# Kernel tuning notes

Measured on AMD Instinct MI355X. Metric: run time of the kernel, lower is better.

The kernel has to match this reference:

```python
import jax, jax.numpy as jnp
import numpy as np

CAPACITY = 0.7
TEMP = 0.5          # initial_temp, never annealed (global_step=None path)
LB_WEIGHT = 0.005
Z_WEIGHT = 5e-06
EPS = 1e-10


def setup_inputs() -> dict:
    key = jax.random.key(0)
    k1, k2, k3 = jax.random.split(key, 3)
    B, S, H = 4, 8192, 2048
    return {
        "hidden_states": jax.random.normal(k1, (B, S, H), dtype=jnp.float32),
        "active_mask": jnp.ones((B, S), dtype=bool),
        "u": jax.random.uniform(k2, (B, S), dtype=jnp.float32),
        # router: nn.Linear(H, 1), weight ~ N(0, 0.02), bias = 0
        "w": jax.random.normal(k3, (H,), dtype=jnp.float32) * 0.02,
        "b": jnp.zeros((), dtype=jnp.float32),
    }


def reference(hidden_states, active_mask, u, w, b):
    B, S = active_mask.shape
    N = B * S
    # mask is all-True by construction -> num_active = N, k static
    num_active = N
    k = max(1, min(int(CAPACITY * num_active), num_active))

    # scores = router(hidden).squeeze(-1)  -> [B,S]
    scores = jnp.einsum("bsh,h->bs", hidden_states, w) + b
    scores = jnp.where(active_mask, scores, -jnp.inf)

    # gumbel noise from uniform u (matches torch.rand_like path)
    gumbel = -jnp.log(-jnp.log(u + EPS) + EPS)
    noisy = ((scores + gumbel) / TEMP).reshape(-1)  # [N]

    _, idx = jax.lax.top_k(noisy, k)
    ffn_mask = jnp.zeros((N,), dtype=bool).at[idx].set(True)
    ffn_mask = ffn_mask.reshape(B, S) & active_mask

    # aux losses (masked reductions over active tokens)
    maskf = active_mask.astype(jnp.float32)
    na = maskf.sum()
    safe_scores = jnp.where(active_mask, scores, 0.0)
    f = ffn_mask.astype(jnp.float32).sum() / na
    p = (jax.nn.sigmoid(safe_scores) * maskf).sum() / na
    lb_loss = (f - CAPACITY) ** 2 + (p - CAPACITY) ** 2
    z_loss = (safe_scores ** 2 * maskf).sum() / na
    aux_loss = LB_WEIGHT * lb_loss + Z_WEIGHT * z_loss

    return ffn_mask, aux_loss
```

## Files before the change

### kernel.cpp

```cpp
#include <hip/hip_runtime.h>
#include <math.h>

#define NTOK 32768
#define HDIM 2048
#define K_SEL 22937
#define EPS_F 1e-10f
#define SBLK 1024

__global__ void zero_kernel(uint4* __restrict__ h4)
{
    h4[blockIdx.x * 256 + threadIdx.x] = make_uint4(0u, 0u, 0u, 0u);
}

__global__ __launch_bounds__(256) void score_kernel(
    const float* __restrict__ hidden,
    const float* __restrict__ u,
    const float* __restrict__ w,
    const float* __restrict__ b,
    unsigned int* __restrict__ keys,
    float* __restrict__ pp,
    float* __restrict__ zz,
    unsigned int* __restrict__ hist,
    int shift)
{
    const int wave = threadIdx.x >> 6;
    const int lane = threadIdx.x & 63;
    const int row0 = blockIdx.x * 32 + wave * 8;

    const float4* __restrict__ w4 = (const float4*)w;
    float4 wr[8];
    #pragma unroll
    for (int j = 0; j < 8; ++j) wr[j] = w4[j * 64 + lane];

    const float4* __restrict__ rowp = (const float4*)(hidden + (size_t)row0 * HDIM);

    float sums[8];
    float4 buf[2][8];
    #pragma unroll
    for (int j = 0; j < 8; ++j) buf[0][j] = rowp[j * 64 + lane];

    #pragma unroll
    for (int r = 0; r < 8; ++r) {
        const int cur = r & 1, nxt = cur ^ 1;
        if (r < 7) {
            #pragma unroll
            for (int j = 0; j < 8; ++j)
                buf[nxt][j] = rowp[(r + 1) * 512 + j * 64 + lane];
        }
        float s = 0.0f;
        #pragma unroll
        for (int j = 0; j < 8; ++j) {
            const float4 hv = buf[cur][j];
            s += hv.x * wr[j].x + hv.y * wr[j].y + hv.z * wr[j].z + hv.w * wr[j].w;
        }
        sums[r] = s;
    }

    #pragma unroll
    for (int off = 32; off > 0; off >>= 1) {
        #pragma unroll
        for (int r = 0; r < 8; ++r)
            sums[r] += __shfl_down(sums[r], off, 64);
    }

    __shared__ float red_p[4], red_z[4];
    if (lane == 0) {
        const float bias = b[0];
        float p_acc = 0.0f, z_acc = 0.0f;
        #pragma unroll
        for (int r = 0; r < 8; ++r) {
            const float score = sums[r] + bias;
            const float uu = u[row0 + r];
            const float g = -logf(-logf(uu + EPS_F) + EPS_F);
            const float noisy = (score + g) * 2.0f;
            const unsigned int bits = __float_as_uint(noisy);
            const unsigned int k = (bits & 0x80000000u) ? ~bits : (bits | 0x80000000u);
            keys[row0 + r] = k;
            atomicAdd(&hist[k >> shift], 1u);
            p_acc += 1.0f / (1.0f + expf(-score));
            z_acc += score * score;
        }
        red_p[wave] = p_acc;
        red_z[wave] = z_acc;
    }
    __syncthreads();
    if (threadIdx.x == 0) {
        pp[blockIdx.x] = red_p[0] + red_p[1] + red_p[2] + red_p[3];
        zz[blockIdx.x] = red_z[0] + red_z[1] + red_z[2] + red_z[3];
    }
}

__global__ __launch_bounds__(1024) void tau_kernel(
    const unsigned int* __restrict__ keys,
    const unsigned int* __restrict__ hist,
    const float* __restrict__ pp,
    const float* __restrict__ zz,
    unsigned int* __restrict__ meta,
    float* __restrict__ out,
    int shift)
{
    __shared__ unsigned int wcnt[16];
    __shared__ int sB;
    __shared__ float wredp[16], wredz[16];

    const int t = threadIdx.x;
    const int lane = t & 63;
    const int wid = t >> 6;
    const int bins = 1 << (32 - shift);
    const int g = bins >> 10;

    unsigned int s = 0;
    if ((g & 3) == 0) {
        const uint4* h4 = (const uint4*)hist;
        const int gq = g >> 2;
        for (int i = 0; i < gq; ++i) {
            const uint4 v = h4[t * gq + i];
            s += v.x + v.y + v.z + v.w;
        }
    } else {
        for (int i = 0; i < g; ++i) s += hist[t * g + i];
    }
    unsigned int suf = s;
    #pragma unroll
    for (int off = 1; off < 64; off <<= 1) {
        const unsigned int n = __shfl_down(suf, off, 64);
        if (lane + off < 64) suf += n;
    }
    if (lane == 0) wcnt[wid] = suf;
    __syncthreads();
    unsigned int hi = 0;
    for (int i = wid + 1; i < 16; ++i) hi += wcnt[i];
    const unsigned int SufT = suf + hi;
    if (SufT >= (unsigned int)K_SEL && SufT - s < (unsigned int)K_SEL) {
        unsigned int run = SufT - s;
        for (int bb = g - 1; bb >= 0; --bb) {
            run += hist[t * g + bb];
            if (run >= (unsigned int)K_SEL) { sB = t * g + bb; break; }
        }
    }
    __syncthreads();
    unsigned int tau = ((unsigned int)sB) << shift;

    uint4 k4[8];
    const uint4* kk4 = (const uint4*)keys;
    #pragma unroll
    for (int j = 0; j < 8; ++j) k4[j] = kk4[1024 * j + t];
    unsigned int myk[32];
    #pragma unroll
    for (int j = 0; j < 8; ++j) {
        myk[4 * j + 0] = k4[j].x;
        myk[4 * j + 1] = k4[j].y;
        myk[4 * j + 2] = k4[j].z;
        myk[4 * j + 3] = k4[j].w;
    }

    auto blocksum = [&](unsigned int c) -> unsigned int {
        #pragma unroll
        for (int off = 32; off > 0; off >>= 1) c += __shfl_down(c, off, 64);
        if (lane == 0) wcnt[wid] = c;
        __syncthreads();
        unsigned int tot = 0;
        #pragma unroll
        for (int i = 0; i < 16; ++i) tot += wcnt[i];
        __syncthreads();
        return tot;
    };

    for (int bit = shift - 1; bit >= 0; --bit) {
        const unsigned int cand = tau | (1u << bit);
        unsigned int c = 0;
        #pragma unroll
        for (int m = 0; m < 32; ++m) c += (myk[m] >= cand) ? 1u : 0u;
        if (blocksum(c) >= (unsigned int)K_SEL) tau = cand;
    }

    unsigned int cgt = 0, ceq = 0;
    #pragma unroll
    for (int m = 0; m < 32; ++m) {
        cgt += (myk[m] > tau) ? 1u : 0u;
        ceq += (myk[m] == tau) ? 1u : 0u;
    }
    const unsigned int totp = blocksum((cgt << 16) | ceq);
    const unsigned int tot_gt = totp >> 16;
    const unsigned int tot_eq = totp & 0xFFFFu;
    const unsigned int needed = (unsigned int)K_SEL - tot_gt;

    unsigned int X = NTOK - 1;
    if (needed < tot_eq) {
        auto cntle = [&](unsigned int cand) -> unsigned int {
            unsigned int c = 0;
            #pragma unroll
            for (int m = 0; m < 32; ++m) {
                const unsigned int idx = 4096u * (m >> 2) + 4u * t + (m & 3);
                c += (myk[m] == tau && idx <= cand) ? 1u : 0u;
            }
            return blocksum(c);
        };
        if (cntle(0) >= needed) {
            X = 0;
        } else {
            unsigned int Y = 0;
            for (int bit = 14; bit >= 0; --bit) {
                const unsigned int cand = Y | (1u << bit);
                if (cntle(cand) < needed) Y = cand;
            }
            X = Y + 1;
        }
    }

    if (t == 0) { meta[0] = tau; meta[1] = X; }

    float lp = pp[t], lz = zz[t];
    #pragma unroll
    for (int off = 32; off > 0; off >>= 1) {
        lp += __shfl_down(lp, off, 64);
        lz += __shfl_down(lz, off, 64);
    }
    if (lane == 0) { wredp[wid] = lp; wredz[wid] = lz; }
    __syncthreads();
    if (t == 0) {
        float sp = 0.0f, sz = 0.0f;
        for (int i = 0; i < 16; ++i) { sp += wredp[i]; sz += wredz[i]; }
        const float na = (float)NTOK;
        const float f = (float)K_SEL / na;
        const float p = sp / na;
        const float z = sz / na;
        const float d1 = f - 0.7f;
        const float d2 = p - 0.7f;
        out[NTOK] = 0.005f * (d1 * d1 + d2 * d2) + 5e-6f * z;
    }
}

__global__ __launch_bounds__(128) void mask_kernel(
    const unsigned int* __restrict__ keys,
    const unsigned int* __restrict__ meta,
    float* __restrict__ out)
{
    const unsigned int tau = meta[0];
    const unsigned int X = meta[1];
    const int i = blockIdx.x * 128 + threadIdx.x;
    const uint4 kv = ((const uint4*)keys)[i];
    const unsigned int e = 4u * (unsigned int)i;
    float4 o;
    o.x = (kv.x > tau || (kv.x == tau && e     <= X)) ? 1.0f : 0.0f;
    o.y = (kv.y > tau || (kv.y == tau && e + 1 <= X)) ? 1.0f : 0.0f;
    o.z = (kv.z > tau || (kv.z == tau && e + 2 <= X)) ? 1.0f : 0.0f;
    o.w = (kv.w > tau || (kv.w == tau && e + 3 <= X)) ? 1.0f : 0.0f;
    ((float4*)out)[i] = o;
}

extern "C" void kernel_launch(void* const* d_in, const int* in_sizes, int n_in,
                              void* d_out, int out_size, void* d_ws, size_t ws_size,
                              hipStream_t stream) {
    const float* hidden = (const float*)d_in[0];
    const float* u = (const float*)d_in[2];
    const float* w = (const float*)d_in[3];
    const float* b = (const float*)d_in[4];
    float* out = (float*)d_out;

    const size_t KEYS_B = (size_t)NTOK * sizeof(unsigned int);
    const size_t PART_B = (size_t)SBLK * sizeof(float);
    const size_t META_B = 256;
    const size_t HIST16 = ((size_t)1 << 16) * sizeof(unsigned int);

    int bits = 16;
    char* wsp = (char*)d_ws;
    unsigned int *keys, *hist, *meta;
    float *pp, *zz;

    if (ws_size >= KEYS_B + 2 * PART_B + HIST16 + META_B) {
        keys = (unsigned int*)wsp;
        pp = (float*)(wsp + KEYS_B);
        zz = pp + SBLK;
        hist = (unsigned int*)(wsp + KEYS_B + 2 * PART_B);
        meta = hist + (1 << 16);
    } else if (ws_size >= 2 * PART_B + HIST16 + META_B) {
        keys = (unsigned int*)d_out;
        pp = (float*)wsp;
        zz = pp + SBLK;
        hist = (unsigned int*)(wsp + 2 * PART_B);
        meta = hist + (1 << 16);
    } else {
        bits = 10;
        keys = (unsigned int*)d_out;
        pp = (float*)wsp;
        zz = pp + SBLK;
        hist = (unsigned int*)(wsp + 2 * PART_B);
        meta = hist + (1 << 10);
    }
    const int shift = 32 - bits;
    const int zblocks = (1 << bits) / 1024;

    zero_kernel<<<zblocks, 256, 0, stream>>>((uint4*)hist);
    score_kernel<<<SBLK, 256, 0, stream>>>(hidden, u, w, b, keys, pp, zz, hist, shift);
    tau_kernel<<<1, 1024, 0, stream>>>(keys, hist, pp, zz, meta, out, shift);
    mask_kernel<<<64, 128, 0, stream>>>(keys, meta, out);
}
```

Measured before the change: 407.5 us.

## Build radix histogram in LDS inside tau kernel, drop global histogram and zero kernel

```diff
diff --git a/kernel.cpp b/kernel.cpp
--- a/kernel.cpp
+++ b/kernel.cpp
@@ -6,11 +6,6 @@
 #define K_SEL 22937
 #define EPS_F 1e-10f
 #define SBLK 1024
-
-__global__ void zero_kernel(uint4* __restrict__ h4)
-{
-    h4[blockIdx.x * 256 + threadIdx.x] = make_uint4(0u, 0u, 0u, 0u);
-}
 
 __global__ __launch_bounds__(256) void score_kernel(
     const float* __restrict__ hidden,
@@ -19,9 +14,7 @@
     const float* __restrict__ b,
     unsigned int* __restrict__ keys,
     float* __restrict__ pp,
-    float* __restrict__ zz,
-    unsigned int* __restrict__ hist,
-    int shift)
+    float* __restrict__ zz)
 {
     const int wave = threadIdx.x >> 6;
     const int lane = threadIdx.x & 63;
@@ -74,9 +67,7 @@
             const float g = -logf(-logf(uu + EPS_F) + EPS_F);
             const float noisy = (score + g) * 2.0f;
             const unsigned int bits = __float_as_uint(noisy);
-            const unsigned int k = (bits & 0x80000000u) ? ~bits : (bits | 0x80000000u);
-            keys[row0 + r] = k;
-            atomicAdd(&hist[k >> shift], 1u);
+            keys[row0 + r] = (bits & 0x80000000u) ? ~bits : (bits | 0x80000000u);
             p_acc += 1.0f / (1.0f + expf(-score));
             z_acc += score * score;
         }
@@ -90,15 +81,17 @@
     }
 }
 
+#define HSHIFT 19
+#define HBINS  (1 << (32 - HSHIFT))
+
 __global__ __launch_bounds__(1024) void tau_kernel(
     const unsigned int* __restrict__ keys,
-    const unsigned int* __restrict__ hist,
     const float* __restrict__ pp,
     const float* __restrict__ zz,
     unsigned int* __restrict__ meta,
-    float* __restrict__ out,
-    int shift)
+    float* __restrict__ out)
 {
+    __shared__ unsigned int shist[HBINS];
     __shared__ unsigned int wcnt[16];
     __shared__ int sB;
     __shared__ float wredp[16], wredz[16];
@@ -106,40 +99,9 @@
     const int t = threadIdx.x;
     const int lane = t & 63;
     const int wid = t >> 6;
-    const int bins = 1 << (32 - shift);
-    const int g = bins >> 10;
-
-    unsigned int s = 0;
-    if ((g & 3) == 0) {
-        const uint4* h4 = (const uint4*)hist;
-        const int gq = g >> 2;
-        for (int i = 0; i < gq; ++i) {
-            const uint4 v = h4[t * gq + i];
-            s += v.x + v.y + v.z + v.w;
-        }
-    } else {
-        for (int i = 0; i < g; ++i) s += hist[t * g + i];
-    }
-    unsigned int suf = s;
-    #pragma unroll
-    for (int off = 1; off < 64; off <<= 1) {
-        const unsigned int n = __shfl_down(suf, off, 64);
-        if (lane + off < 64) suf += n;
-    }
-    if (lane == 0) wcnt[wid] = suf;
-    __syncthreads();
-    unsigned int hi = 0;
-    for (int i = wid + 1; i < 16; ++i) hi += wcnt[i];
-    const unsigned int SufT = suf + hi;
-    if (SufT >= (unsigned int)K_SEL && SufT - s < (unsigned int)K_SEL) {
-        unsigned int run = SufT - s;
-        for (int bb = g - 1; bb >= 0; --bb) {
-            run += hist[t * g + bb];
-            if (run >= (unsigned int)K_SEL) { sB = t * g + bb; break; }
-        }
-    }
-    __syncthreads();
-    unsigned int tau = ((unsigned int)sB) << shift;
+
+    #pragma unroll
+    for (int i = 0; i < HBINS / 1024; ++i) shist[t * (HBINS / 1024) + i] = 0u;
 
     uint4 k4[8];
     const uint4* kk4 = (const uint4*)keys;
@@ -153,6 +115,38 @@
         myk[4 * j + 2] = k4[j].z;
         myk[4 * j + 3] = k4[j].w;
     }
+    __syncthreads();
+
+    #pragma unroll
+    for (int m = 0; m < 32; ++m) atomicAdd(&shist[myk[m] >> HSHIFT], 1u);
+    __syncthreads();
+
+    {
+        const int g = HBINS / 1024;
+        unsigned int s = 0;
+        #pragma unroll
+        for (int i = 0; i < g; ++i) s += shist[t * g + i];
+        unsigned int suf = s;
+        #pragma unroll
+        for (int off = 1; off < 64; off <<= 1) {
+            const unsigned int n = __shfl_down(suf, off, 64);
+            if (lane + off < 64) suf += n;
+        }
+        if (lane == 0) wcnt[wid] = suf;
+        __syncthreads();
+        unsigned int hi = 0;
+        for (int i = wid + 1; i < 16; ++i) hi += wcnt[i];
+        const unsigned int SufT = suf + hi;
+        if (SufT >= (unsigned int)K_SEL && SufT - s < (unsigned int)K_SEL) {
+            unsigned int run = SufT - s;
+            for (int bb = g - 1; bb >= 0; --bb) {
+                run += shist[t * g + bb];
+                if (run >= (unsigned int)K_SEL) { sB = t * g + bb; break; }
+            }
+        }
+        __syncthreads();
+    }
+    unsigned int tau = ((unsigned int)sB) << HSHIFT;
 
     auto blocksum = [&](unsigned int c) -> unsigned int {
         #pragma unroll
@@ -166,7 +160,7 @@
         return tot;
     };
 
-    for (int bit = shift - 1; bit >= 0; --bit) {
+    for (int bit = HSHIFT - 1; bit >= 0; --bit) {
         const unsigned int cand = tau | (1u << bit);
         unsigned int c = 0;
         #pragma unroll
@@ -261,38 +255,24 @@
     const size_t KEYS_B = (size_t)NTOK * sizeof(unsigned int);
     const size_t PART_B = (size_t)SBLK * sizeof(float);
     const size_t META_B = 256;
-    const size_t HIST16 = ((size_t)1 << 16) * sizeof(unsigned int);
-
-    int bits = 16;
+
     char* wsp = (char*)d_ws;
-    unsigned int *keys, *hist, *meta;
+    unsigned int *keys, *meta;
     float *pp, *zz;
 
-    if (ws_size >= KEYS_B + 2 * PART_B + HIST16 + META_B) {
+    if (ws_size >= KEYS_B + 2 * PART_B + META_B) {
         keys = (unsigned int*)wsp;
         pp = (float*)(wsp + KEYS_B);
         zz = pp + SBLK;
-        hist = (unsigned int*)(wsp + KEYS_B + 2 * PART_B);
-        meta = hist + (1 << 16);
-    } else if (ws_size >= 2 * PART_B + HIST16 + META_B) {
+        meta = (unsigned int*)(wsp + KEYS_B + 2 * PART_B);
+    } else {
         keys = (unsigned int*)d_out;
         pp = (float*)wsp;
         zz = pp + SBLK;
-        hist = (unsigned int*)(wsp + 2 * PART_B);
-        meta = hist + (1 << 16);
-    } else {
-        bits = 10;
-        keys = (unsigned int*)d_out;
-        pp = (float*)wsp;
-        zz = pp + SBLK;
-        hist = (unsigned int*)(wsp + 2 * PART_B);
-        meta = hist + (1 << 10);
-    }
-    const int shift = 32 - bits;
-    const int zblocks = (1 << bits) / 1024;
-
-    zero_kernel<<<zblocks, 256, 0, stream>>>((uint4*)hist);
-    score_kernel<<<SBLK, 256, 0, stream>>>(hidden, u, w, b, keys, pp, zz, hist, shift);
-    tau_kernel<<<1, 1024, 0, stream>>>(keys, hist, pp, zz, meta, out, shift);
+        meta = (unsigned int*)(wsp + 2 * PART_B);
+    }
+
+    score_kernel<<<SBLK, 256, 0, stream>>>(hidden, u, w, b, keys, pp, zz);
+    tau_kernel<<<1, 1024, 0, stream>>>(keys, pp, zz, meta, out);
     mask_kernel<<<64, 128, 0, stream>>>(keys, meta, out);
 }
```

New measurement: 394.6 us. -3.2%, faster.
